# Kernel optimization log

Hardware: AMD Instinct MI355X
Metric: run time of the kernel (lower is better)

## Reference

```python
import jax, jax.numpy as jnp
import numpy as np

# dims
N = 50000          # nodes
E = 400000         # edges
R = 32             # radial basis
F = 132            # features_dim
EV = 15            # sum(2l+1) for degrees [1,2,3]
H_INV, D_INV = 4, 33
H_EV, D_EV = 3, 44
REPEATS = np.array([3, 5, 7])            # 2l+1 per degree
ATT_NORM_INV = float(np.sqrt(D_INV))
ATT_NORM_EV = float(np.sqrt(D_EV))

# degree contraction matrix: (x*x) @ M sums squared m-components per degree -> [.., 3]
M_L0 = np.zeros((EV, 3), np.float32)
_off = 0
for _i, _r in enumerate(REPEATS):
    M_L0[_off:_off + _r, _i] = 1.0
    _off += _r
M_L0 = jnp.asarray(M_L0)


def _filter_net(rbf, ev_inv, rW1, rb1, rW2, rb2, eW1, eb1, eW2, eb2):
    # FilterNet with num_layers=2: silu(Linear) -> Linear(identity), same for ev path
    a = jax.nn.silu(rbf @ rW1 + rb1) @ rW2 + rb2
    e = jax.nn.silu(ev_inv @ eW1 + eb1) @ eW2 + eb2
    return a + e


def setup_inputs() -> dict:
    key = jax.random.key(0)
    ks = jax.random.split(key, 40)
    p = lambda i, shp, s=0.1: jax.random.normal(ks[i], shp, jnp.float32) * s
    inp = {
        'inv_features': jax.random.normal(ks[0], (N, F), jnp.float32),
        'ev_features': jax.random.normal(ks[1], (N, EV), jnp.float32),
        'rbf': jax.random.uniform(ks[2], (E, R), jnp.float32),
        'sh_vectors': jax.random.normal(ks[3], (E, EV), jnp.float32),
        'cutoffs': jax.random.uniform(ks[4], (E, 1), jnp.float32),
        'senders': jax.random.randint(ks[5], (E,), 0, N),
        'receivers': jax.random.randint(ks[6], (E,), 0, N),
        # attention weights
        'Wq_inv': p(7, (H_INV, D_INV, D_INV)),
        'Wk_inv': p(8, (H_INV, D_INV, D_INV)),
        'Wv_inv': p(9, (H_INV, D_INV, D_INV)),
        'Wq_ev': p(10, (H_EV, D_EV, D_EV)),
        'Wk_ev': p(11, (H_EV, D_EV, D_EV)),
        # filter net (inv branch)
        'fi_rW1': p(12, (R, F)), 'fi_rb1': p(13, (F,)),
        'fi_rW2': p(14, (F, F)), 'fi_rb2': p(15, (F,)),
        'fi_eW1': p(16, (3, F // 4)), 'fi_eb1': p(17, (F // 4,)),
        'fi_eW2': p(18, (F // 4, F)), 'fi_eb2': p(19, (F,)),
        # filter net (ev branch)
        'fe_rW1': p(20, (R, F)), 'fe_rb1': p(21, (F,)),
        'fe_rW2': p(22, (F, F)), 'fe_rb2': p(23, (F,)),
        'fe_eW1': p(24, (3, F // 4)), 'fe_eb1': p(25, (F // 4,)),
        'fe_eW2': p(26, (F // 4, F)), 'fe_eb2': p(27, (F,)),
        # interaction block linear: (F + len(degrees)) -> (F + len(degrees))
        'W_int': p(28, (F + 3, F + 3)), 'b_int': p(29, (F + 3,)),
    }
    return inp


def reference(inv_features, ev_features, rbf, sh_vectors, cutoffs,
              Wq_inv, Wk_inv, Wv_inv, Wq_ev, Wk_ev,
              fi_rW1, fi_rb1, fi_rW2, fi_rb2, fi_eW1, fi_eb1, fi_eW2, fi_eb2,
              fe_rW1, fe_rb1, fe_rW2, fe_rb2, fe_eW1, fe_eb1, fe_eW2, fe_eb2,
              W_int, b_int, senders, receivers):
    n = inv_features.shape[0]

    # --- Euclidean attention block ---
    ev_diff = ev_features[senders] - ev_features[receivers]          # [E, 15]
    ev_diff_inv = (ev_diff * ev_diff) @ M_L0                          # [E, 3] L0 contraction

    fw_inv = _filter_net(rbf, ev_diff_inv, fi_rW1, fi_rb1, fi_rW2, fi_rb2,
                         fi_eW1, fi_eb1, fi_eW2, fi_eb2).reshape(-1, H_INV, D_INV)
    fw_ev = _filter_net(rbf, ev_diff_inv, fe_rW1, fe_rb1, fe_rW2, fe_rb2,
                        fe_eW1, fe_eb1, fe_eW2, fe_eb2).reshape(-1, H_EV, D_EV)

    x_inv = inv_features.reshape(n, H_INV, D_INV)
    x_ev = inv_features.reshape(n, H_EV, D_EV)

    q_inv = jax.nn.silu(jnp.einsum('nhd,hde->nhe', x_inv, Wq_inv))[receivers]
    k_inv = jax.nn.silu(jnp.einsum('nhd,hde->nhe', x_inv, Wk_inv))[senders]
    v_inv = jnp.einsum('nhd,hde->nhe', x_inv, Wv_inv)[senders]
    q_ev = jax.nn.silu(jnp.einsum('nhd,hde->nhe', x_ev, Wq_ev))[receivers]
    k_ev = jax.nn.silu(jnp.einsum('nhd,hde->nhe', x_ev, Wk_ev))[senders]

    alpha_inv = (q_inv * k_inv * fw_inv).sum(-1) / ATT_NORM_INV       # [E, 4]
    alpha_ev = (q_ev * k_ev * fw_ev).sum(-1) / ATT_NORM_EV            # [E, 3]

    msg_inv = cutoffs[:, :, None] * alpha_inv[..., None] * v_inv      # [E, 4, 33]
    d_inv = jax.ops.segment_sum(msg_inv, receivers, num_segments=n).reshape(n, F)

    alpha_ev_full = jnp.repeat(alpha_ev, REPEATS, axis=-1, total_repeat_length=EV)
    msg_ev = cutoffs * alpha_ev_full * sh_vectors                      # [E, 15]
    d_ev = jax.ops.segment_sum(msg_ev, receivers, num_segments=n)

    inv1 = inv_features + d_inv
    ev1 = ev_features + d_ev

    # --- Interaction block ---
    ev1_inv = (ev1 * ev1) @ M_L0                                       # [N, 3]
    t = jnp.concatenate([inv1, ev1_inv], axis=-1) @ W_int + b_int      # [N, 135]
    d_inv2, b_ev = t[:, :F], t[:, F:]
    d_ev2 = jnp.repeat(b_ev, REPEATS, axis=-1, total_repeat_length=EV) * ev1

    return (inv1 + d_inv2, ev1 + d_ev2)
```

## Files before the change

kernel.cpp:

```cpp
#include <hip/hip_runtime.h>
#include <type_traits>

#define N_NODES 50000
#define N_EDGES 400000
#define R_DIM   32
#define F_DIM   132
#define EV_DIM  15
#define F_Q     33
#define INT_DIM 135
#define TE      32
#define NPB     32

#define RCP_NORM_INV 0.17407765595569785f
#define RCP_NORM_EV  0.15075567228888181f

typedef __attribute__((ext_vector_type(8))) short bf16x8;
typedef __attribute__((ext_vector_type(4))) float f32x4;

__device__ __forceinline__ float silu_f(float x) {
    return x * __builtin_amdgcn_rcpf(1.f + __expf(-x));
}

__device__ __forceinline__ unsigned short f2bf(float x) {
    union { float f; unsigned u; } c; c.f = x;
    unsigned r = c.u + 0x7FFFu + ((c.u >> 16) & 1u);
    return (unsigned short)(r >> 16);
}

__device__ __forceinline__ float bf2f(unsigned short x) {
    union { unsigned u; float f; } c; c.u = (unsigned)x << 16;
    return c.f;
}

__global__ __launch_bounds__(256) void prep_w2_kernel(
    const float* __restrict__ fi_rW2, const float* __restrict__ fi_eW2,
    const float* __restrict__ fe_rW2, const float* __restrict__ fe_eW2,
    const float* __restrict__ fi_rb2, const float* __restrict__ fi_eb2,
    const float* __restrict__ fe_rb2, const float* __restrict__ fe_eb2,
    const float* __restrict__ W_int,
    unsigned short* __restrict__ Bfrag, float* __restrict__ biasC,
    unsigned short* __restrict__ Wfrag_int)
{
    int t = blockIdx.x * 256 + threadIdx.x;
    if (t < 6912) {
        int l = t & 63, idx = t >> 6;
        int nt = idx % 9, kc = (idx / 9) % 6, f = idx / 54;
        const float* rW2 = f ? fe_rW2 : fi_rW2;
        const float* eW2 = f ? fe_eW2 : fi_eW2;
        int n = nt * 16 + (l & 15);
        unsigned short v[8];
        #pragma unroll
        for (int j = 0; j < 8; ++j) {
            int k = kc * 32 + (l >> 4) * 8 + j;
            float w = 0.f;
            if (n < F_DIM) {
                if (k < F_DIM) w = rW2[k * F_DIM + n];
                else if (k < F_DIM + F_Q) w = eW2[(k - F_DIM) * F_DIM + n];
            }
            v[j] = f2bf(w);
        }
        *(uint4*)&Bfrag[(size_t)t * 8] = *(const uint4*)v;
    } else if (t < 6912 + 2880) {
        int u = t - 6912;
        int l = u & 63, idx = u >> 6;
        int nt = idx % 9, kc = idx / 9;
        int n = nt * 16 + (l & 15);
        unsigned short v[8];
        #pragma unroll
        for (int j = 0; j < 8; ++j) {
            int k = kc * 32 + (l >> 4) * 8 + j;
            float w = (k < INT_DIM && n < INT_DIM) ? W_int[k * INT_DIM + n] : 0.f;
            v[j] = f2bf(w);
        }
        *(uint4*)&Wfrag_int[(size_t)u * 8] = *(const uint4*)v;
    }
    if (blockIdx.x == 0) {
        for (int i = threadIdx.x; i < 288; i += 256) {
            int f = i / 144, n = i % 144;
            const float* rb2 = f ? fe_rb2 : fi_rb2;
            const float* eb2 = f ? fe_eb2 : fi_eb2;
            biasC[i] = (n < F_DIM) ? (rb2[n] + eb2[n]) : 0.f;
        }
    }
}

__global__ __launch_bounds__(256) void prep_aux_kernel(
    const float* __restrict__ fi_rW1, const float* __restrict__ fe_rW1,
    const float* __restrict__ fi_rb1, const float* __restrict__ fi_eb1,
    const float* __restrict__ fe_rb1, const float* __restrict__ fe_eb1,
    const float* __restrict__ Wq_inv, const float* __restrict__ Wk_inv,
    const float* __restrict__ Wv_inv,
    const float* __restrict__ Wq_ev, const float* __restrict__ Wk_ev,
    unsigned short* __restrict__ B1frag, float* __restrict__ biasB1,
    unsigned short* __restrict__ Bnp)
{
    int t = blockIdx.x * 256 + threadIdx.x;
    if (t < 1536) {
        int l = t & 63, idx = t >> 6;
        int nt = idx % 12, f = idx / 12;
        const float* rW1 = f ? fe_rW1 : fi_rW1;
        int n = nt * 16 + (l & 15);
        unsigned short v[8];
        #pragma unroll
        for (int j = 0; j < 8; ++j) {
            int k = (l >> 4) * 8 + j;
            float w = (n < F_DIM) ? rW1[k * F_DIM + n] : 0.f;
            v[j] = f2bf(w);
        }
        *(uint4*)&B1frag[(size_t)t * 8] = *(const uint4*)v;
    } else if (t < 1920) {
        int i = t - 1536;
        int f = i / 192, n = i % 192;
        const float* rb1 = f ? fe_rb1 : fi_rb1;
        const float* eb1 = f ? fe_eb1 : fi_eb1;
        biasB1[i] = (n < F_DIM) ? rb1[n] : ((n < 165) ? eb1[n - F_DIM] : 0.f);
    } else if (t < 1920 + 6912) {
        int u = t - 1920;
        int l = u & 63, blk = u >> 6;
        int n = 0; const float* W = nullptr; int D = 0, h = 0, kc = 0;
        if (blk < 72) {
            int arr = blk / 24, wb = blk % 24;
            h = wb / 6; kc = (wb % 6) / 3; int nt = wb % 3;
            W = (arr == 0) ? Wq_inv : (arr == 1) ? Wk_inv : Wv_inv;
            D = 33; n = nt * 16 + (l & 15);
            W += h * 1089;
        } else {
            int b2 = blk - 72;
            int which = b2 / 18, wb = b2 % 18;
            h = wb / 6; kc = (wb % 6) / 3; int nt = wb % 3;
            W = which ? Wk_ev : Wq_ev;
            D = 44; n = nt * 16 + (l & 15);
            W += h * 1936;
        }
        unsigned short v[8];
        #pragma unroll
        for (int j = 0; j < 8; ++j) {
            int k = kc * 32 + (l >> 4) * 8 + j;
            float w = (k < D && n < D) ? W[k * D + n] : 0.f;
            v[j] = f2bf(w);
        }
        *(uint4*)&Bnp[(size_t)u * 8] = *(const uint4*)v;
    }
}

__global__ __launch_bounds__(256) void hist_kernel(
    const int* __restrict__ receivers, int* __restrict__ cnt)
{
    int i = blockIdx.x * 256 + threadIdx.x;
    if (i < N_EDGES) atomicAdd(&cnt[receivers[i]], 1);
}

__global__ __launch_bounds__(1024) void scan_tile_sum(
    const int* __restrict__ cnt, int* __restrict__ tsum)
{
    int idx = blockIdx.x * 1024 + threadIdx.x;
    int v = (idx < N_NODES) ? cnt[idx] : 0;
    for (int o = 32; o > 0; o >>= 1) v += __shfl_down(v, o);
    __shared__ int wsum[16];
    if ((threadIdx.x & 63) == 0) wsum[threadIdx.x >> 6] = v;
    __syncthreads();
    if (threadIdx.x == 0) {
        int s = 0;
        for (int i = 0; i < 16; ++i) s += wsum[i];
        tsum[blockIdx.x] = s;
    }
}

__global__ __launch_bounds__(64) void scan_base(
    const int* __restrict__ tsum, int* __restrict__ tbase)
{
    if (threadIdx.x == 0) {
        int run = 0;
        for (int i = 0; i < 49; ++i) { tbase[i] = run; run += tsum[i]; }
    }
}

__global__ __launch_bounds__(1024) void scan_tile(
    const int* __restrict__ cnt, const int* __restrict__ tbase,
    int* __restrict__ off, int* __restrict__ cursor)
{
    __shared__ int s[1024];
    int t = threadIdx.x;
    int idx = blockIdx.x * 1024 + t;
    int v = (idx < N_NODES) ? cnt[idx] : 0;
    s[t] = v;
    __syncthreads();
    for (int d = 1; d < 1024; d <<= 1) {
        int x = (t >= d) ? s[t - d] : 0;
        __syncthreads();
        s[t] += x;
        __syncthreads();
    }
    int o = tbase[blockIdx.x] + s[t] - v;
    if (idx < N_NODES) { off[idx] = o; cursor[idx] = o; }
    if (idx == 0) off[N_NODES] = N_EDGES;
}

__global__ __launch_bounds__(256) void scatter_kernel(
    const int* __restrict__ receivers, int* __restrict__ cursor,
    int* __restrict__ perm)
{
    int i = blockIdx.x * 256 + threadIdx.x;
    if (i < N_EDGES) {
        int pos = atomicAdd(&cursor[receivers[i]], 1);
        perm[pos] = i;
    }
}

__global__ __launch_bounds__(256) void node_proj_kernel(
    const float* __restrict__ x,
    const unsigned short* __restrict__ Bnp,
    unsigned short* __restrict__ q_inv, unsigned short* __restrict__ k_inv,
    unsigned short* __restrict__ v_bf,
    unsigned short* __restrict__ q_ev, unsigned short* __restrict__ k_ev)
{
    __shared__ __align__(16) unsigned short sx[NPB][456];
    const int node0 = blockIdx.x * NPB;
    const int tid = threadIdx.x;
    for (int i = tid; i < NPB * 448; i += 256) {
        int nd = i / 448, t = i % 448;
        int seg = t >> 6, d = t & 63;
        float v = 0.f;
        int gn = node0 + nd;
        if (gn < N_NODES) {
            if (seg < 4) { if (d < 33) v = x[(size_t)gn * F_DIM + seg * 33 + d]; }
            else         { int h = seg - 4; if (d < 44) v = x[(size_t)gn * F_DIM + h * 44 + d]; }
        }
        sx[nd][t] = f2bf(v);
    }
    __syncthreads();
    const int wv = tid >> 6, l = tid & 63, l15 = l & 15, g4 = l >> 4;
    const int half = wv & 1, m0 = (wv >> 1) * 16;
    const unsigned short* arow = &sx[m0 + l15][0];
    const unsigned short* Bl = Bnp + (size_t)l * 8;

    auto do_inv = [&](int arr, unsigned short* __restrict__ out, bool dosilu) {
        const unsigned short* Ba = Bl + (size_t)arr * 24 * 512;
        #pragma unroll
        for (int h = 0; h < 4; ++h) {
            bf16x8 a0 = *(const bf16x8*)&arow[h * 64 + g4 * 8];
            bf16x8 a1 = *(const bf16x8*)&arow[h * 64 + 32 + g4 * 8];
            #pragma unroll
            for (int nt = 0; nt < 3; ++nt) {
                f32x4 c = {0.f, 0.f, 0.f, 0.f};
                c = __builtin_amdgcn_mfma_f32_16x16x32_bf16(
                        a0, *(const bf16x8*)(Ba + (size_t)((h * 2 + 0) * 3 + nt) * 512), c, 0, 0, 0);
                c = __builtin_amdgcn_mfma_f32_16x16x32_bf16(
                        a1, *(const bf16x8*)(Ba + (size_t)((h * 2 + 1) * 3 + nt) * 512), c, 0, 0, 0);
                int e = nt * 16 + l15;
                if (e < 33) {
                    #pragma unroll
                    for (int r = 0; r < 4; ++r) {
                        int gn = node0 + m0 + g4 * 4 + r;
                        if (gn < N_NODES) {
                            float v = c[r];
                            if (dosilu) v = silu_f(v);
                            out[(size_t)gn * F_DIM + h * 33 + e] = f2bf(v);
                        }
                    }
                }
            }
        }
    };
    auto do_ev = [&](int which, unsigned short* __restrict__ out) {
        const unsigned short* Ba = Bl + (size_t)(72 + which * 18) * 512;
        #pragma unroll
        for (int h = 0; h < 3; ++h) {
            bf16x8 a0 = *(const bf16x8*)&arow[256 + h * 64 + g4 * 8];
            bf16x8 a1 = *(const bf16x8*)&arow[256 + h * 64 + 32 + g4 * 8];
            #pragma unroll
            for (int nt = 0; nt < 3; ++nt) {
                f32x4 c = {0.f, 0.f, 0.f, 0.f};
                c = __builtin_amdgcn_mfma_f32_16x16x32_bf16(
                        a0, *(const bf16x8*)(Ba + (size_t)((h * 2 + 0) * 3 + nt) * 512), c, 0, 0, 0);
                c = __builtin_amdgcn_mfma_f32_16x16x32_bf16(
                        a1, *(const bf16x8*)(Ba + (size_t)((h * 2 + 1) * 3 + nt) * 512), c, 0, 0, 0);
                int e = nt * 16 + l15;
                if (e < 44) {
                    #pragma unroll
                    for (int r = 0; r < 4; ++r) {
                        int gn = node0 + m0 + g4 * 4 + r;
                        if (gn < N_NODES)
                            out[(size_t)gn * F_DIM + h * 44 + e] = f2bf(silu_f(c[r]));
                    }
                }
            }
        }
    };
    if (half == 0) { do_inv(0, q_inv, true); do_inv(1, k_inv, true); }
    else           { do_inv(2, v_bf, false); do_ev(0, q_ev); do_ev(1, k_ev); }
}

__global__ __launch_bounds__(256) void edge_alpha_kernel(
    const float* __restrict__ ev_feat, const float* __restrict__ rbf,
    const float* __restrict__ cutoffs,
    const int* __restrict__ senders, const int* __restrict__ receivers,
    const int* __restrict__ perm,
    const float* __restrict__ fi_eW1, const float* __restrict__ fe_eW1,
    const unsigned short* __restrict__ B1frag, const float* __restrict__ biasB1,
    const unsigned short* __restrict__ Bfrag, const float* __restrict__ biasC,
    const unsigned short* __restrict__ q_inv, const unsigned short* __restrict__ k_inv,
    const unsigned short* __restrict__ q_ev, const unsigned short* __restrict__ k_ev,
    float* __restrict__ galpha, int* __restrict__ gsnd)
{
    __shared__ __align__(16) unsigned short s_hid[2][TE][200];
    __shared__ __align__(16) unsigned short s_ain[TE][40];
    __shared__ float s_d2[TE][16];
    __shared__ float s_ei[3][TE];
    __shared__ float s_c[TE];
    __shared__ int s_snd[TE], s_rcv[TE], s_eid[TE];

    const int e0g = blockIdx.x * TE;
    const int tid = threadIdx.x;

    if (tid < TE) {
        int eid = perm[e0g + tid];
        s_eid[tid] = eid;
        int sn = senders[eid], rc = receivers[eid];
        s_snd[tid] = sn; s_rcv[tid] = rc;
        s_c[tid] = cutoffs[eid];
        gsnd[e0g + tid] = sn;
    }
    __syncthreads();
    for (int i = tid; i < TE * R_DIM; i += 256) {
        int e = i >> 5, k = i & 31;
        s_ain[e][k] = f2bf(rbf[(size_t)s_eid[e] * R_DIM + k]);
    }
    for (int i = tid; i < TE * EV_DIM; i += 256) {
        int e = i / EV_DIM, j = i - e * EV_DIM;
        float d = ev_feat[(size_t)s_snd[e] * EV_DIM + j]
                - ev_feat[(size_t)s_rcv[e] * EV_DIM + j];
        s_d2[e][j] = d * d;
    }
    __syncthreads();
    if (tid < TE * 3) {
        int e = tid / 3, k2 = tid - e * 3;
        int i0 = (k2 == 0) ? 0 : (k2 == 1) ? 3 : 8;
        int i1 = (k2 == 0) ? 3 : (k2 == 1) ? 8 : 15;
        float s = 0.f;
        for (int i = i0; i < i1; ++i) s += s_d2[e][i];
        s_ei[k2][e] = s;
    }
    __syncthreads();

    const int wv = tid >> 6, l = tid & 63;
    const int f = wv & 1, m0 = (wv >> 1) * 16;
    const int l15 = l & 15, g4 = l >> 4;

    int rcvr[4], sndr[4];
    #pragma unroll
    for (int r = 0; r < 4; ++r) {
        int e = m0 + g4 * 4 + r;
        rcvr[r] = s_rcv[e]; sndr[r] = s_snd[e];
    }

    {
        bf16x8 a1 = *(const bf16x8*)&s_ain[m0 + l15][g4 * 8];
        const unsigned short* B1f = B1frag + (size_t)f * 6144 + (size_t)l * 8;
        const float* eW1f = f ? fe_eW1 : fi_eW1;
        #pragma unroll
        for (int nt = 0; nt < 12; ++nt) {
            f32x4 c = {0.f, 0.f, 0.f, 0.f};
            bf16x8 b1 = *(const bf16x8*)(B1f + (size_t)nt * 512);
            c = __builtin_amdgcn_mfma_f32_16x16x32_bf16(a1, b1, c, 0, 0, 0);
            const int n = nt * 16 + l15;
            const float bias = biasB1[f * 192 + n];
            float w0 = 0.f, w1 = 0.f, w2 = 0.f;
            if (n >= F_DIM && n < 165) {
                w0 = eW1f[n - F_DIM];
                w1 = eW1f[F_Q + n - F_DIM];
                w2 = eW1f[2 * F_Q + n - F_DIM];
            }
            #pragma unroll
            for (int r = 0; r < 4; ++r) {
                int e = m0 + g4 * 4 + r;
                float eic = w0 * s_ei[0][e] + w1 * s_ei[1][e] + w2 * s_ei[2][e];
                float v = silu_f(c[r] + bias + eic);
                s_hid[f][e][n] = f2bf(v);
            }
        }
    }

    bf16x8 afr[6];
    {
        const unsigned short* hrow = &s_hid[f][m0 + l15][0];
        #pragma unroll
        for (int kc = 0; kc < 6; ++kc)
            afr[kc] = *(const bf16x8*)&hrow[kc * 32 + g4 * 8];
    }
    const unsigned short* Bf = Bfrag + (size_t)f * 54 * 512 + (size_t)l * 8;

    auto run = [&](auto FC) {
        constexpr int F_ = decltype(FC)::value;
        constexpr int NH = F_ ? 3 : 4;
        constexpr int DD = F_ ? 44 : 33;
        const unsigned short* qp = F_ ? q_ev : q_inv;
        const unsigned short* kp = F_ ? k_ev : k_inv;
        float part[NH][4];
        #pragma unroll
        for (int h = 0; h < NH; ++h)
            #pragma unroll
            for (int r = 0; r < 4; ++r) part[h][r] = 0.f;

        auto ldtile = [&](int nt, float (&bq)[4], float (&bk)[4]) {
            const int n = nt * 16 + l15;
            #pragma unroll
            for (int r = 0; r < 4; ++r) {
                float qv = 0.f, kv = 0.f;
                if (n < F_DIM) {
                    qv = bf2f(qp[(size_t)rcvr[r] * F_DIM + n]);
                    kv = bf2f(kp[(size_t)sndr[r] * F_DIM + n]);
                }
                bq[r] = qv; bk[r] = kv;
            }
        };

        float bq[2][4], bk[2][4];
        ldtile(0, bq[0], bk[0]);
        ldtile(1, bq[1], bk[1]);

        #pragma unroll
        for (int nt = 0; nt < 9; ++nt) {
            float cq[4], ck[4];
            #pragma unroll
            for (int r = 0; r < 4; ++r) { cq[r] = bq[nt & 1][r]; ck[r] = bk[nt & 1][r]; }
            if (nt + 2 < 9) ldtile(nt + 2, bq[nt & 1], bk[nt & 1]);

            f32x4 acc = {0.f, 0.f, 0.f, 0.f};
            #pragma unroll
            for (int kc = 0; kc < 6; ++kc) {
                bf16x8 bfr = *(const bf16x8*)(Bf + (size_t)(kc * 9 + nt) * 512);
                acc = __builtin_amdgcn_mfma_f32_16x16x32_bf16(afr[kc], bfr, acc, 0, 0, 0);
            }
            const int n = nt * 16 + l15;
            const bool nvalid = (n < F_DIM);
            const float bias = biasC[F_ * 144 + n];
            int h0v = (nt * 16) / DD;
            int bsp = (h0v + 1) * DD - nt * 16;
            #pragma unroll
            for (int r = 0; r < 4; ++r) {
                float p = 0.f;
                if (nvalid) p = (acc[r] + bias) * cq[r] * ck[r];
                if (bsp >= 16) {
                    part[h0v][r] += p;
                } else {
                    float plo = (l15 < bsp) ? p : 0.f;
                    part[h0v][r] += plo;
                    if (h0v + 1 < NH) part[h0v + 1][r] += (p - plo);
                }
            }
        }
        #pragma unroll
        for (int h = 0; h < NH; ++h) {
            #pragma unroll
            for (int r = 0; r < 4; ++r) {
                float v = part[h][r];
                v += __shfl_xor(v, 1);
                v += __shfl_xor(v, 2);
                v += __shfl_xor(v, 4);
                v += __shfl_xor(v, 8);
                if (l15 == 0) {
                    int e = m0 + g4 * 4 + r;
                    galpha[(size_t)(e0g + e) * 8 + (F_ ? 4 + h : h)] =
                        v * s_c[e] * (F_ ? RCP_NORM_EV : RCP_NORM_INV);
                }
            }
        }
    };
    if (f == 0) run(std::integral_constant<int, 0>{});
    else        run(std::integral_constant<int, 1>{});
}

__global__ __launch_bounds__(256) void gather_kernel(
    const unsigned short* __restrict__ v_bf, const float* __restrict__ sh_vec,
    const float* __restrict__ galpha,
    const int* __restrict__ gsnd, const int* __restrict__ perm,
    const int* __restrict__ off,
    float* __restrict__ a_inv, float* __restrict__ a_ev)
{
    int n = blockIdx.x * 4 + (threadIdx.x >> 6);
    int l = threadIdx.x & 63;
    int beg = off[n], end = off[n + 1];
    int c0 = l, c1 = l + 64, c2 = l + 128;
    int h0 = c0 / 33, h1 = c1 / 33;
    float acc0 = 0.f, acc1 = 0.f, acc2 = 0.f, aev = 0.f;
    int seg = (l < 3) ? 0 : (l < 8) ? 1 : 2;
    #pragma unroll 4
    for (int p = beg; p < end; ++p) {
        int snd = gsnd[p];
        const float* ga = &galpha[(size_t)p * 8];
        const unsigned short* vr = &v_bf[(size_t)snd * F_DIM];
        acc0 += ga[h0] * bf2f(vr[c0]);
        acc1 += ga[h1] * bf2f(vr[c1]);
        if (l < 4) acc2 += ga[3] * bf2f(vr[c2]);
        if (l < EV_DIM) {
            int eid = perm[p];
            aev += ga[4 + seg] * sh_vec[(size_t)eid * EV_DIM + l];
        }
    }
    float* dr = &a_inv[(size_t)n * F_DIM];
    dr[c0] = acc0; dr[c1] = acc1;
    if (l < 4) dr[c2] = acc2;
    if (l < EV_DIM) a_ev[(size_t)n * EV_DIM + l] = aev;
}

__global__ __launch_bounds__(256) void epilogue_kernel(
    const float* __restrict__ inv_feat, const float* __restrict__ ev_feat,
    const float* __restrict__ acc_inv, const float* __restrict__ acc_ev,
    const unsigned short* __restrict__ Wfrag_int, const float* __restrict__ b_int,
    float* __restrict__ out0, float* __restrict__ out1)
{
    const int NB = 16;
    __shared__ float s_in[NB][INT_DIM + 1];
    __shared__ __align__(16) unsigned short s_inb[NB][168];
    __shared__ float s_ev1[NB][EV_DIM + 1];
    __shared__ float s_b[NB][3];
    int n0 = blockIdx.x * NB;
    int tid = threadIdx.x;
    for (int i = tid; i < NB * F_DIM; i += 256) {
        int nb = i / F_DIM, j = i - nb * F_DIM;
        size_t idx = (size_t)(n0 + nb) * F_DIM + j;
        s_in[nb][j] = inv_feat[idx] + acc_inv[idx];
    }
    for (int i = tid; i < NB * EV_DIM; i += 256) {
        int nb = i / EV_DIM, j = i - nb * EV_DIM;
        size_t idx = (size_t)(n0 + nb) * EV_DIM + j;
        s_ev1[nb][j] = ev_feat[idx] + acc_ev[idx];
    }
    __syncthreads();
    if (tid < NB * 3) {
        int nb = tid / 3, k = tid - nb * 3;
        int i0 = (k == 0) ? 0 : (k == 1) ? 3 : 8;
        int i1 = (k == 0) ? 3 : (k == 1) ? 8 : 15;
        float s = 0.f;
        for (int i = i0; i < i1; ++i) { float v = s_ev1[nb][i]; s += v * v; }
        s_in[nb][F_DIM + k] = s;
    }
    __syncthreads();
    for (int i = tid; i < NB * 160; i += 256) {
        int nb = i / 160, j = i - nb * 160;
        s_inb[nb][j] = f2bf((j < INT_DIM) ? s_in[nb][j] : 0.f);
    }
    __syncthreads();
    const int wv = tid >> 6, l = tid & 63, l15 = l & 15, g4 = l >> 4;
    for (int nt = wv; nt < 9; nt += 4) {
        f32x4 c = {0.f, 0.f, 0.f, 0.f};
        #pragma unroll
        for (int kc = 0; kc < 5; ++kc) {
            bf16x8 a = *(const bf16x8*)&s_inb[l15][kc * 32 + g4 * 8];
            bf16x8 b = *(const bf16x8*)(Wfrag_int + (size_t)((kc * 9 + nt) * 64 + l) * 8);
            c = __builtin_amdgcn_mfma_f32_16x16x32_bf16(a, b, c, 0, 0, 0);
        }
        int j = nt * 16 + l15;
        float bias = (j < INT_DIM) ? b_int[j] : 0.f;
        #pragma unroll
        for (int r = 0; r < 4; ++r) {
            int nb = g4 * 4 + r;
            float val = c[r] + bias;
            if (j < F_DIM)
                out0[(size_t)(n0 + nb) * F_DIM + j] = s_in[nb][j] + val;
            else if (j < INT_DIM)
                s_b[nb][j - F_DIM] = val;
        }
    }
    __syncthreads();
    for (int i = tid; i < NB * EV_DIM; i += 256) {
        int nb = i / EV_DIM, ii = i - nb * EV_DIM;
        int seg = (ii < 3) ? 0 : (ii < 8) ? 1 : 2;
        out1[(size_t)(n0 + nb) * EV_DIM + ii] = s_ev1[nb][ii] * (1.f + s_b[nb][seg]);
    }
}

extern "C" void kernel_launch(void* const* d_in, const int* in_sizes, int n_in,
                              void* d_out, int out_size, void* d_ws, size_t ws_size,
                              hipStream_t stream)
{
    const float* inv_feat  = (const float*)d_in[0];
    const float* ev_feat   = (const float*)d_in[1];
    const float* rbf       = (const float*)d_in[2];
    const float* sh_vec    = (const float*)d_in[3];
    const float* cutoffs   = (const float*)d_in[4];
    const int*   senders   = (const int*)d_in[5];
    const int*   receivers = (const int*)d_in[6];
    const float* Wq_inv = (const float*)d_in[7];
    const float* Wk_inv = (const float*)d_in[8];
    const float* Wv_inv = (const float*)d_in[9];
    const float* Wq_ev  = (const float*)d_in[10];
    const float* Wk_ev  = (const float*)d_in[11];
    const float* fi_rW1 = (const float*)d_in[12];
    const float* fi_rb1 = (const float*)d_in[13];
    const float* fi_rW2 = (const float*)d_in[14];
    const float* fi_rb2 = (const float*)d_in[15];
    const float* fi_eW1 = (const float*)d_in[16];
    const float* fi_eb1 = (const float*)d_in[17];
    const float* fi_eW2 = (const float*)d_in[18];
    const float* fi_eb2 = (const float*)d_in[19];
    const float* fe_rW1 = (const float*)d_in[20];
    const float* fe_rb1 = (const float*)d_in[21];
    const float* fe_rW2 = (const float*)d_in[22];
    const float* fe_rb2 = (const float*)d_in[23];
    const float* fe_eW1 = (const float*)d_in[24];
    const float* fe_eb1 = (const float*)d_in[25];
    const float* fe_eW2 = (const float*)d_in[26];
    const float* fe_eb2 = (const float*)d_in[27];
    const float* W_int  = (const float*)d_in[28];
    const float* b_int  = (const float*)d_in[29];

    const size_t NF = (size_t)N_NODES * F_DIM;
    const size_t NE = (size_t)N_NODES * EV_DIM;
    float* ws    = (float*)d_ws;
    float* a_inv = ws;
    float* a_ev  = ws + NF;
    float* galpha = a_ev + NE;
    int*   perm   = (int*)(galpha + (size_t)N_EDGES * 8);
    int*   gsnd   = perm + N_EDGES;
    int*   cnt    = gsnd + N_EDGES;
    int*   off    = cnt + N_NODES;
    int*   cursor = off + (N_NODES + 4);
    unsigned short* Bfrag  = (unsigned short*)(cursor + N_NODES);
    float*          biasC  = (float*)(Bfrag + 55296);
    unsigned short* B1frag = (unsigned short*)(biasC + 288);
    float*          biasB1 = (float*)(B1frag + 12288);
    unsigned short* Bnp    = (unsigned short*)(biasB1 + 384);
    int* tsum  = (int*)(Bnp + 55296);
    int* tbase = tsum + 64;
    unsigned short* q_inv = (unsigned short*)(tbase + 64);
    unsigned short* k_inv = q_inv + NF;
    unsigned short* q_ev  = k_inv + NF;
    unsigned short* k_ev  = q_ev + NF;
    unsigned short* v_bf  = k_ev + NF;
    unsigned short* Wfrag_int = v_bf + NF;

    float* out0 = (float*)d_out;
    float* out1 = out0 + NF;

    hipMemsetAsync(cnt, 0, N_NODES * sizeof(int), stream);
    hist_kernel<<<(N_EDGES + 255) / 256, 256, 0, stream>>>(receivers, cnt);
    scan_tile_sum<<<49, 1024, 0, stream>>>(cnt, tsum);
    scan_base<<<1, 64, 0, stream>>>(tsum, tbase);
    scan_tile<<<49, 1024, 0, stream>>>(cnt, tbase, off, cursor);
    scatter_kernel<<<(N_EDGES + 255) / 256, 256, 0, stream>>>(receivers, cursor, perm);

    prep_w2_kernel<<<39, 256, 0, stream>>>(
        fi_rW2, fi_eW2, fe_rW2, fe_eW2,
        fi_rb2, fi_eb2, fe_rb2, fe_eb2, W_int, Bfrag, biasC, Wfrag_int);

    prep_aux_kernel<<<35, 256, 0, stream>>>(
        fi_rW1, fe_rW1, fi_rb1, fi_eb1, fe_rb1, fe_eb1,
        Wq_inv, Wk_inv, Wv_inv, Wq_ev, Wk_ev,
        B1frag, biasB1, Bnp);

    node_proj_kernel<<<(N_NODES + NPB - 1) / NPB, 256, 0, stream>>>(
        inv_feat, Bnp, q_inv, k_inv, v_bf, q_ev, k_ev);

    edge_alpha_kernel<<<N_EDGES / TE, 256, 0, stream>>>(
        ev_feat, rbf, cutoffs, senders, receivers, perm,
        fi_eW1, fe_eW1, B1frag, biasB1, Bfrag, biasC,
        q_inv, k_inv, q_ev, k_ev,
        galpha, gsnd);

    gather_kernel<<<N_NODES / 4, 256, 0, stream>>>(
        v_bf, sh_vec, galpha, gsnd, perm, off, a_inv, a_ev);

    epilogue_kernel<<<N_NODES / 16, 256, 0, stream>>>(
        inv_feat, ev_feat, a_inv, a_ev, Wfrag_int, b_int, out0, out1);
}
```

Before: 720.0 us.

## Fuse gather into epilogue, merge prep kernels, and fold scan base into scan

The per-node gather of weighted sender values now happens inside the epilogue kernel and writes straight into shared memory. This removes the a_inv/a_ev round trip through global memory and one launch. The two weight-prep kernels are merged into one launch, and the serial scan_base kernel is dropped: each scan_tile block sums the earlier tile totals itself. The cost is that each epilogue block handles 16 nodes with 4 waves looping sequentially over 4 nodes each, so the block has less gather parallelism than the old one-node-per-wave kernel.

```diff
diff --git a/kernel.cpp b/kernel.cpp
--- a/kernel.cpp
+++ b/kernel.cpp
@@ -32,59 +32,14 @@
     return c.f;
 }
 
-__global__ __launch_bounds__(256) void prep_w2_kernel(
+__global__ __launch_bounds__(256) void prep_kernel(
     const float* __restrict__ fi_rW2, const float* __restrict__ fi_eW2,
     const float* __restrict__ fe_rW2, const float* __restrict__ fe_eW2,
     const float* __restrict__ fi_rb2, const float* __restrict__ fi_eb2,
     const float* __restrict__ fe_rb2, const float* __restrict__ fe_eb2,
     const float* __restrict__ W_int,
     unsigned short* __restrict__ Bfrag, float* __restrict__ biasC,
-    unsigned short* __restrict__ Wfrag_int)
-{
-    int t = blockIdx.x * 256 + threadIdx.x;
-    if (t < 6912) {
-        int l = t & 63, idx = t >> 6;
-        int nt = idx % 9, kc = (idx / 9) % 6, f = idx / 54;
-        const float* rW2 = f ? fe_rW2 : fi_rW2;
-        const float* eW2 = f ? fe_eW2 : fi_eW2;
-        int n = nt * 16 + (l & 15);
-        unsigned short v[8];
-        #pragma unroll
-        for (int j = 0; j < 8; ++j) {
-            int k = kc * 32 + (l >> 4) * 8 + j;
-            float w = 0.f;
-            if (n < F_DIM) {
-                if (k < F_DIM) w = rW2[k * F_DIM + n];
-                else if (k < F_DIM + F_Q) w = eW2[(k - F_DIM) * F_DIM + n];
-            }
-            v[j] = f2bf(w);
-        }
-        *(uint4*)&Bfrag[(size_t)t * 8] = *(const uint4*)v;
-    } else if (t < 6912 + 2880) {
-        int u = t - 6912;
-        int l = u & 63, idx = u >> 6;
-        int nt = idx % 9, kc = idx / 9;
-        int n = nt * 16 + (l & 15);
-        unsigned short v[8];
-        #pragma unroll
-        for (int j = 0; j < 8; ++j) {
-            int k = kc * 32 + (l >> 4) * 8 + j;
-            float w = (k < INT_DIM && n < INT_DIM) ? W_int[k * INT_DIM + n] : 0.f;
-            v[j] = f2bf(w);
-        }
-        *(uint4*)&Wfrag_int[(size_t)u * 8] = *(const uint4*)v;
-    }
-    if (blockIdx.x == 0) {
-        for (int i = threadIdx.x; i < 288; i += 256) {
-            int f = i / 144, n = i % 144;
-            const float* rb2 = f ? fe_rb2 : fi_rb2;
-            const float* eb2 = f ? fe_eb2 : fi_eb2;
-            biasC[i] = (n < F_DIM) ? (rb2[n] + eb2[n]) : 0.f;
-        }
-    }
-}
-
-__global__ __launch_bounds__(256) void prep_aux_kernel(
+    unsigned short* __restrict__ Wfrag_int,
     const float* __restrict__ fi_rW1, const float* __restrict__ fe_rW1,
     const float* __restrict__ fi_rb1, const float* __restrict__ fi_eb1,
     const float* __restrict__ fe_rb1, const float* __restrict__ fe_eb1,
@@ -94,52 +49,96 @@
     unsigned short* __restrict__ B1frag, float* __restrict__ biasB1,
     unsigned short* __restrict__ Bnp)
 {
-    int t = blockIdx.x * 256 + threadIdx.x;
-    if (t < 1536) {
-        int l = t & 63, idx = t >> 6;
-        int nt = idx % 12, f = idx / 12;
-        const float* rW1 = f ? fe_rW1 : fi_rW1;
-        int n = nt * 16 + (l & 15);
-        unsigned short v[8];
-        #pragma unroll
-        for (int j = 0; j < 8; ++j) {
-            int k = (l >> 4) * 8 + j;
-            float w = (n < F_DIM) ? rW1[k * F_DIM + n] : 0.f;
-            v[j] = f2bf(w);
-        }
-        *(uint4*)&B1frag[(size_t)t * 8] = *(const uint4*)v;
-    } else if (t < 1920) {
-        int i = t - 1536;
-        int f = i / 192, n = i % 192;
-        const float* rb1 = f ? fe_rb1 : fi_rb1;
-        const float* eb1 = f ? fe_eb1 : fi_eb1;
-        biasB1[i] = (n < F_DIM) ? rb1[n] : ((n < 165) ? eb1[n - F_DIM] : 0.f);
-    } else if (t < 1920 + 6912) {
-        int u = t - 1920;
-        int l = u & 63, blk = u >> 6;
-        int n = 0; const float* W = nullptr; int D = 0, h = 0, kc = 0;
-        if (blk < 72) {
-            int arr = blk / 24, wb = blk % 24;
-            h = wb / 6; kc = (wb % 6) / 3; int nt = wb % 3;
-            W = (arr == 0) ? Wq_inv : (arr == 1) ? Wk_inv : Wv_inv;
-            D = 33; n = nt * 16 + (l & 15);
-            W += h * 1089;
-        } else {
-            int b2 = blk - 72;
-            int which = b2 / 18, wb = b2 % 18;
-            h = wb / 6; kc = (wb % 6) / 3; int nt = wb % 3;
-            W = which ? Wk_ev : Wq_ev;
-            D = 44; n = nt * 16 + (l & 15);
-            W += h * 1936;
-        }
-        unsigned short v[8];
-        #pragma unroll
-        for (int j = 0; j < 8; ++j) {
-            int k = kc * 32 + (l >> 4) * 8 + j;
-            float w = (k < D && n < D) ? W[k * D + n] : 0.f;
-            v[j] = f2bf(w);
-        }
-        *(uint4*)&Bnp[(size_t)u * 8] = *(const uint4*)v;
+    if (blockIdx.x < 39) {
+        int t = blockIdx.x * 256 + threadIdx.x;
+        if (t < 6912) {
+            int l = t & 63, idx = t >> 6;
+            int nt = idx % 9, kc = (idx / 9) % 6, f = idx / 54;
+            const float* rW2 = f ? fe_rW2 : fi_rW2;
+            const float* eW2 = f ? fe_eW2 : fi_eW2;
+            int n = nt * 16 + (l & 15);
+            unsigned short v[8];
+            #pragma unroll
+            for (int j = 0; j < 8; ++j) {
+                int k = kc * 32 + (l >> 4) * 8 + j;
+                float w = 0.f;
+                if (n < F_DIM) {
+                    if (k < F_DIM) w = rW2[k * F_DIM + n];
+                    else if (k < F_DIM + F_Q) w = eW2[(k - F_DIM) * F_DIM + n];
+                }
+                v[j] = f2bf(w);
+            }
+            *(uint4*)&Bfrag[(size_t)t * 8] = *(const uint4*)v;
+        } else if (t < 6912 + 2880) {
+            int u = t - 6912;
+            int l = u & 63, idx = u >> 6;
+            int nt = idx % 9, kc = idx / 9;
+            int n = nt * 16 + (l & 15);
+            unsigned short v[8];
+            #pragma unroll
+            for (int j = 0; j < 8; ++j) {
+                int k = kc * 32 + (l >> 4) * 8 + j;
+                float w = (k < INT_DIM && n < INT_DIM) ? W_int[k * INT_DIM + n] : 0.f;
+                v[j] = f2bf(w);
+            }
+            *(uint4*)&Wfrag_int[(size_t)u * 8] = *(const uint4*)v;
+        }
+        if (blockIdx.x == 0) {
+            for (int i = threadIdx.x; i < 288; i += 256) {
+                int f = i / 144, n = i % 144;
+                const float* rb2 = f ? fe_rb2 : fi_rb2;
+                const float* eb2 = f ? fe_eb2 : fi_eb2;
+                biasC[i] = (n < F_DIM) ? (rb2[n] + eb2[n]) : 0.f;
+            }
+        }
+    } else {
+        int t = (blockIdx.x - 39) * 256 + threadIdx.x;
+        if (t < 1536) {
+            int l = t & 63, idx = t >> 6;
+            int nt = idx % 12, f = idx / 12;
+            const float* rW1 = f ? fe_rW1 : fi_rW1;
+            int n = nt * 16 + (l & 15);
+            unsigned short v[8];
+            #pragma unroll
+            for (int j = 0; j < 8; ++j) {
+                int k = (l >> 4) * 8 + j;
+                float w = (n < F_DIM) ? rW1[k * F_DIM + n] : 0.f;
+                v[j] = f2bf(w);
+            }
+            *(uint4*)&B1frag[(size_t)t * 8] = *(const uint4*)v;
+        } else if (t < 1920) {
+            int i = t - 1536;
+            int f = i / 192, n = i % 192;
+            const float* rb1 = f ? fe_rb1 : fi_rb1;
+            const float* eb1 = f ? fe_eb1 : fi_eb1;
+            biasB1[i] = (n < F_DIM) ? rb1[n] : ((n < 165) ? eb1[n - F_DIM] : 0.f);
+        } else if (t < 1920 + 6912) {
+            int u = t - 1920;
+            int l = u & 63, blk = u >> 6;
+            int n = 0; const float* W = nullptr; int D = 0, h = 0, kc = 0;
+            if (blk < 72) {
+                int arr = blk / 24, wb = blk % 24;
+                h = wb / 6; kc = (wb % 6) / 3; int nt = wb % 3;
+                W = (arr == 0) ? Wq_inv : (arr == 1) ? Wk_inv : Wv_inv;
+                D = 33; n = nt * 16 + (l & 15);
+                W += h * 1089;
+            } else {
+                int b2 = blk - 72;
+                int which = b2 / 18, wb = b2 % 18;
+                h = wb / 6; kc = (wb % 6) / 3; int nt = wb % 3;
+                W = which ? Wk_ev : Wq_ev;
+                D = 44; n = nt * 16 + (l & 15);
+                W += h * 1936;
+            }
+            unsigned short v[8];
+            #pragma unroll
+            for (int j = 0; j < 8; ++j) {
+                int k = kc * 32 + (l >> 4) * 8 + j;
+                float w = (k < D && n < D) ? W[k * D + n] : 0.f;
+                v[j] = f2bf(w);
+            }
+            *(uint4*)&Bnp[(size_t)u * 8] = *(const uint4*)v;
+        }
     }
 }
 
@@ -166,21 +165,18 @@
     }
 }
 
-__global__ __launch_bounds__(64) void scan_base(
-    const int* __restrict__ tsum, int* __restrict__ tbase)
-{
-    if (threadIdx.x == 0) {
-        int run = 0;
-        for (int i = 0; i < 49; ++i) { tbase[i] = run; run += tsum[i]; }
-    }
-}
-
 __global__ __launch_bounds__(1024) void scan_tile(
-    const int* __restrict__ cnt, const int* __restrict__ tbase,
+    const int* __restrict__ cnt, const int* __restrict__ tsum,
     int* __restrict__ off, int* __restrict__ cursor)
 {
     __shared__ int s[1024];
+    __shared__ int sbase;
     int t = threadIdx.x;
+    if (t == 0) {
+        int b = 0;
+        for (int i = 0; i < (int)blockIdx.x; ++i) b += tsum[i];
+        sbase = b;
+    }
     int idx = blockIdx.x * 1024 + t;
     int v = (idx < N_NODES) ? cnt[idx] : 0;
     s[t] = v;
@@ -191,7 +187,7 @@
         s[t] += x;
         __syncthreads();
     }
-    int o = tbase[blockIdx.x] + s[t] - v;
+    int o = sbase + s[t] - v;
     if (idx < N_NODES) { off[idx] = o; cursor[idx] = o; }
     if (idx == 0) off[N_NODES] = N_EDGES;
 }
@@ -471,42 +467,12 @@
     else        run(std::integral_constant<int, 1>{});
 }
 
-__global__ __launch_bounds__(256) void gather_kernel(
+__global__ __launch_bounds__(256) void fused_gather_epilogue(
+    const float* __restrict__ inv_feat, const float* __restrict__ ev_feat,
     const unsigned short* __restrict__ v_bf, const float* __restrict__ sh_vec,
     const float* __restrict__ galpha,
     const int* __restrict__ gsnd, const int* __restrict__ perm,
     const int* __restrict__ off,
-    float* __restrict__ a_inv, float* __restrict__ a_ev)
-{
-    int n = blockIdx.x * 4 + (threadIdx.x >> 6);
-    int l = threadIdx.x & 63;
-    int beg = off[n], end = off[n + 1];
-    int c0 = l, c1 = l + 64, c2 = l + 128;
-    int h0 = c0 / 33, h1 = c1 / 33;
-    float acc0 = 0.f, acc1 = 0.f, acc2 = 0.f, aev = 0.f;
-    int seg = (l < 3) ? 0 : (l < 8) ? 1 : 2;
-    #pragma unroll 4
-    for (int p = beg; p < end; ++p) {
-        int snd = gsnd[p];
-        const float* ga = &galpha[(size_t)p * 8];
-        const unsigned short* vr = &v_bf[(size_t)snd * F_DIM];
-        acc0 += ga[h0] * bf2f(vr[c0]);
-        acc1 += ga[h1] * bf2f(vr[c1]);
-        if (l < 4) acc2 += ga[3] * bf2f(vr[c2]);
-        if (l < EV_DIM) {
-            int eid = perm[p];
-            aev += ga[4 + seg] * sh_vec[(size_t)eid * EV_DIM + l];
-        }
-    }
-    float* dr = &a_inv[(size_t)n * F_DIM];
-    dr[c0] = acc0; dr[c1] = acc1;
-    if (l < 4) dr[c2] = acc2;
-    if (l < EV_DIM) a_ev[(size_t)n * EV_DIM + l] = aev;
-}
-
-__global__ __launch_bounds__(256) void epilogue_kernel(
-    const float* __restrict__ inv_feat, const float* __restrict__ ev_feat,
-    const float* __restrict__ acc_inv, const float* __restrict__ acc_ev,
     const unsigned short* __restrict__ Wfrag_int, const float* __restrict__ b_int,
     float* __restrict__ out0, float* __restrict__ out1)
 {
@@ -517,17 +483,40 @@
     __shared__ float s_b[NB][3];
     int n0 = blockIdx.x * NB;
     int tid = threadIdx.x;
-    for (int i = tid; i < NB * F_DIM; i += 256) {
-        int nb = i / F_DIM, j = i - nb * F_DIM;
-        size_t idx = (size_t)(n0 + nb) * F_DIM + j;
-        s_in[nb][j] = inv_feat[idx] + acc_inv[idx];
-    }
-    for (int i = tid; i < NB * EV_DIM; i += 256) {
-        int nb = i / EV_DIM, j = i - nb * EV_DIM;
-        size_t idx = (size_t)(n0 + nb) * EV_DIM + j;
-        s_ev1[nb][j] = ev_feat[idx] + acc_ev[idx];
-    }
-    __syncthreads();
+    const int wv = tid >> 6, l = tid & 63;
+
+    {
+        int c0 = l, c1 = l + 64, c2 = l + 128;
+        int h0 = c0 / 33, h1 = c1 / 33;
+        int seg = (l < 3) ? 0 : (l < 8) ? 1 : 2;
+        for (int nl = 0; nl < 4; ++nl) {
+            int nb = wv * 4 + nl;
+            int n = n0 + nb;
+            int beg = off[n], end = off[n + 1];
+            float acc0 = 0.f, acc1 = 0.f, acc2 = 0.f, aev = 0.f;
+            #pragma unroll 4
+            for (int p = beg; p < end; ++p) {
+                int snd = gsnd[p];
+                const float* ga = &galpha[(size_t)p * 8];
+                const unsigned short* vr = &v_bf[(size_t)snd * F_DIM];
+                acc0 += ga[h0] * bf2f(vr[c0]);
+                acc1 += ga[h1] * bf2f(vr[c1]);
+                if (l < 4) acc2 += ga[3] * bf2f(vr[c2]);
+                if (l < EV_DIM) {
+                    int eid = perm[p];
+                    aev += ga[4 + seg] * sh_vec[(size_t)eid * EV_DIM + l];
+                }
+            }
+            size_t base = (size_t)n * F_DIM;
+            s_in[nb][c0] = inv_feat[base + c0] + acc0;
+            s_in[nb][c1] = inv_feat[base + c1] + acc1;
+            if (l < 4) s_in[nb][c2] = inv_feat[base + c2] + acc2;
+            if (l < EV_DIM)
+                s_ev1[nb][l] = ev_feat[(size_t)n * EV_DIM + l] + aev;
+        }
+    }
+    __syncthreads();
+
     if (tid < NB * 3) {
         int nb = tid / 3, k = tid - nb * 3;
         int i0 = (k == 0) ? 0 : (k == 1) ? 3 : 8;
@@ -542,7 +531,7 @@
         s_inb[nb][j] = f2bf((j < INT_DIM) ? s_in[nb][j] : 0.f);
     }
     __syncthreads();
-    const int wv = tid >> 6, l = tid & 63, l15 = l & 15, g4 = l >> 4;
+    const int l15 = l & 15, g4 = l >> 4;
     for (int nt = wv; nt < 9; nt += 4) {
         f32x4 c = {0.f, 0.f, 0.f, 0.f};
         #pragma unroll
@@ -607,11 +596,8 @@
     const float* b_int  = (const float*)d_in[29];
 
     const size_t NF = (size_t)N_NODES * F_DIM;
-    const size_t NE = (size_t)N_NODES * EV_DIM;
     float* ws    = (float*)d_ws;
-    float* a_inv = ws;
-    float* a_ev  = ws + NF;
-    float* galpha = a_ev + NE;
+    float* galpha = ws;
     int*   perm   = (int*)(galpha + (size_t)N_EDGES * 8);
     int*   gsnd   = perm + N_EDGES;
     int*   cnt    = gsnd + N_EDGES;
@@ -623,8 +609,7 @@
     float*          biasB1 = (float*)(B1frag + 12288);
     unsigned short* Bnp    = (unsigned short*)(biasB1 + 384);
     int* tsum  = (int*)(Bnp + 55296);
-    int* tbase = tsum + 64;
-    unsigned short* q_inv = (unsigned short*)(tbase + 64);
+    unsigned short* q_inv = (unsigned short*)(tsum + 64);
     unsigned short* k_inv = q_inv + NF;
     unsigned short* q_ev  = k_inv + NF;
     unsigned short* k_ev  = q_ev + NF;
@@ -637,15 +622,12 @@
     hipMemsetAsync(cnt, 0, N_NODES * sizeof(int), stream);
     hist_kernel<<<(N_EDGES + 255) / 256, 256, 0, stream>>>(receivers, cnt);
     scan_tile_sum<<<49, 1024, 0, stream>>>(cnt, tsum);
-    scan_base<<<1, 64, 0, stream>>>(tsum, tbase);
-    scan_tile<<<49, 1024, 0, stream>>>(cnt, tbase, off, cursor);
+    scan_tile<<<49, 1024, 0, stream>>>(cnt, tsum, off, cursor);
     scatter_kernel<<<(N_EDGES + 255) / 256, 256, 0, stream>>>(receivers, cursor, perm);
 
-    prep_w2_kernel<<<39, 256, 0, stream>>>(
+    prep_kernel<<<74, 256, 0, stream>>>(
         fi_rW2, fi_eW2, fe_rW2, fe_eW2,
-        fi_rb2, fi_eb2, fe_rb2, fe_eb2, W_int, Bfrag, biasC, Wfrag_int);
-
-    prep_aux_kernel<<<35, 256, 0, stream>>>(
+        fi_rb2, fi_eb2, fe_rb2, fe_eb2, W_int, Bfrag, biasC, Wfrag_int,
         fi_rW1, fe_rW1, fi_rb1, fi_eb1, fe_rb1, fe_eb1,
         Wq_inv, Wk_inv, Wv_inv, Wq_ev, Wk_ev,
         B1frag, biasB1, Bnp);
@@ -659,9 +641,7 @@
         q_inv, k_inv, q_ev, k_ev,
         galpha, gsnd);
 
-    gather_kernel<<<N_NODES / 4, 256, 0, stream>>>(
-        v_bf, sh_vec, galpha, gsnd, perm, off, a_inv, a_ev);
-
-    epilogue_kernel<<<N_NODES / 16, 256, 0, stream>>>(
-        inv_feat, ev_feat, a_inv, a_ev, Wfrag_int, b_int, out0, out1);
-}
+    fused_gather_epilogue<<<N_NODES / 16, 256, 0, stream>>>(
+        inv_feat, ev_feat, v_bf, sh_vec, galpha, gsnd, perm, off,
+        Wfrag_int, b_int, out0, out1);
+}
```

Result: no change. 722.1 us (+0.3%).
